# Kernel tuning notes

Hardware: AMD Instinct MI355X
Metric: run time of the kernel (lower is better)

## Reference

```python
import jax, jax.numpy as jnp
import numpy as np

H = 16  # num_heads
D = 1024  # hidden_size

def setup_inputs() -> dict:
    key = jax.random.key(0)
    ks = jax.random.split(key, 9)
    s = 1.0 / np.sqrt(D).astype(np.float32)
    return {
        'x':  jax.random.normal(ks[0], (2, 2048, D), dtype=jnp.float32),
        'wq': jax.random.normal(ks[1], (D, D), dtype=jnp.float32) * s,
        'bq': jax.random.normal(ks[2], (D,), dtype=jnp.float32) * s,
        'wk': jax.random.normal(ks[3], (D, D), dtype=jnp.float32) * s,
        'bk': jax.random.normal(ks[4], (D,), dtype=jnp.float32) * s,
        'wv': jax.random.normal(ks[5], (D, D), dtype=jnp.float32) * s,
        'bv': jax.random.normal(ks[6], (D,), dtype=jnp.float32) * s,
        'wo': jax.random.normal(ks[7], (D, D), dtype=jnp.float32) * s,
        'bo': jax.random.normal(ks[8], (D,), dtype=jnp.float32) * s,
    }

def _split_heads(t):
    # [b, s, (h d)] -> [b, h, s, d]
    b, s, _ = t.shape
    return t.reshape(b, s, H, D // H).transpose(0, 2, 1, 3)

def reference(x, wq, bq, wk, bk, wv, bv, wo, bo):
    q = _split_heads(x @ wq + bq)  # [b, h, s, d]
    k = _split_heads(x @ wk + bk)
    v = _split_heads(x @ wv + bv)
    scale = 1.0 / jnp.sqrt(jnp.asarray(q.shape[-1], q.dtype))
    attn = jnp.einsum('bhqd,bhkd->bhqk', q, k) * scale
    attn = jax.nn.softmax(attn, axis=-1)
    o = jnp.einsum('bhqk,bhkd->bhqd', attn, v)
    b, h, s, d = o.shape
    o = o.transpose(0, 2, 1, 3).reshape(b, s, h * d)  # concat heads
    return o @ wo + bo
```

## Files before the change

kernel.cpp:

```cpp
#include <hip/hip_runtime.h>
#include <stdint.h>
#include <stddef.h>


typedef __bf16 bf16_t;
typedef __bf16 bf16x8 __attribute__((ext_vector_type(8)));
typedef __bf16 bf16x4 __attribute__((ext_vector_type(4)));
typedef __bf16 bf16x2 __attribute__((ext_vector_type(2)));
typedef float  f32x4  __attribute__((ext_vector_type(4)));
typedef float  f32x8  __attribute__((ext_vector_type(8)));
typedef float  f32x16 __attribute__((ext_vector_type(16)));
typedef uint32_t u32x4 __attribute__((ext_vector_type(4)));

static constexpr float kQScale = 0.18033688011112042f;

__device__ __forceinline__ void gload_lds16(const bf16_t* g, bf16_t* l) {
  __builtin_amdgcn_global_load_lds((__attribute__((address_space(1))) void*)(void*)g,
                                   (__attribute__((address_space(3))) void*)l, 16, 0, 0);
}

__device__ __forceinline__ uint32_t pk_bf16(float lo, float hi) {
  bf16x2 v; v[0] = (bf16_t)lo; v[1] = (bf16_t)hi;
  return __builtin_bit_cast(uint32_t, v);
}

__global__ __launch_bounds__(256) void prep_k(
    const float* __restrict__ x, bf16_t* __restrict__ xb,
    const float* __restrict__ wq, const float* __restrict__ wk,
    const float* __restrict__ wv, const float* __restrict__ wo,
    bf16_t* __restrict__ wqkvT, bf16_t* __restrict__ woT) {
  __shared__ float t[64][65];
  const int z = blockIdx.z;
  if (z == 4) {
    const int blk = blockIdx.y * 16 + blockIdx.x;
#pragma unroll
    for (int c = 0; c < 16; ++c) {
      const int i = c * 65536 + blk * 256 + threadIdx.x;
      float4 v = ((const float4*)x)[i];
      bf16x4 o;
      o[0] = (bf16_t)v.x; o[1] = (bf16_t)v.y; o[2] = (bf16_t)v.z; o[3] = (bf16_t)v.w;
      ((bf16x4*)xb)[i] = o;
    }
    return;
  }
  const float* src = z == 0 ? wq : z == 1 ? wk : z == 2 ? wv : wo;
  bf16_t* dst = z < 3 ? wqkvT + (size_t)z * 1024 * 1024 : woT;
  int n0 = blockIdx.x * 64, k0 = blockIdx.y * 64;
  int c = threadIdx.x & 63, r4 = threadIdx.x >> 6;
#pragma unroll
  for (int i = 0; i < 16; ++i) {
    int r = r4 + i * 4;
    t[r][c] = src[(size_t)(k0 + r) * 1024 + (n0 + c)];
  }
  __syncthreads();
#pragma unroll
  for (int i = 0; i < 16; ++i) {
    int r = r4 + i * 4;
    dst[(size_t)(n0 + r) * 1024 + (k0 + c)] = (bf16_t)t[c][r];
  }
}

__global__ __launch_bounds__(256) void gemm_qkv_k(
    const bf16_t* __restrict__ A, const bf16_t* __restrict__ Bw,
    bf16_t* __restrict__ Qb, bf16_t* __restrict__ Kb, bf16_t* __restrict__ Vt,
    const float* __restrict__ bq, const float* __restrict__ bk, const float* __restrict__ bv) {
  __shared__ alignas(16) bf16_t As[128 * 32];
  __shared__ alignas(16) bf16_t Bs[128 * 32];
  const int tid = threadIdx.x;
  const int lane = tid & 63;
  const int w = tid >> 6, wr = w >> 1, wc = w & 1;
  const int brow = blockIdx.y * 128, bcol = blockIdx.x * 128;
  const int l15 = lane & 15, ko = (lane >> 4) * 8;

  f32x4 acc[4][4] = {};
  const bf16_t* Ab = A + (size_t)brow * 1024;
  const bf16_t* Bb = Bw + (size_t)bcol * 1024;

  const int e0 = tid * 8;
  const int r0 = e0 >> 5, c0 = e0 & 31;

  for (int k0 = 0; k0 < 1024; k0 += 32) {
    gload_lds16(Ab + (size_t)r0 * 1024 + k0 + c0, &As[e0]);
    gload_lds16(Ab + (size_t)(r0 + 64) * 1024 + k0 + c0, &As[e0 + 2048]);
    gload_lds16(Bb + (size_t)r0 * 1024 + k0 + c0, &Bs[e0]);
    gload_lds16(Bb + (size_t)(r0 + 64) * 1024 + k0 + c0, &Bs[e0 + 2048]);
    __syncthreads();
    bf16x8 af[4], bfg[4];
#pragma unroll
    for (int i = 0; i < 4; ++i)
      af[i] = *(const bf16x8*)&As[(wr * 64 + i * 16 + l15) * 32 + ko];
#pragma unroll
    for (int i = 0; i < 4; ++i)
      bfg[i] = *(const bf16x8*)&Bs[(wc * 64 + i * 16 + l15) * 32 + ko];
#pragma unroll
    for (int i = 0; i < 4; ++i)
#pragma unroll
      for (int j = 0; j < 4; ++j)
        acc[i][j] = __builtin_amdgcn_mfma_f32_16x16x32_bf16(af[i], bfg[j], acc[i][j], 0, 0, 0);
    __syncthreads();
  }

  const int mat = bcol >> 10;
#pragma unroll
  for (int i = 0; i < 4; ++i) {
    const int gm0 = brow + wr * 64 + i * 16 + ((lane >> 4) << 2);
    const int b = gm0 >> 11, s0 = gm0 & 2047;
#pragma unroll
    for (int j = 0; j < 4; ++j) {
      const int gn = bcol + wc * 64 + j * 16 + l15;
      const int col = gn & 1023;
      const int h = col >> 6, dd = col & 63;
      if (mat == 2) {
        const float bsv = bv[col];
        bf16x4 pk;
#pragma unroll
        for (int r = 0; r < 4; ++r) pk[r] = (bf16_t)(acc[i][j][r] + bsv);
        *(bf16x4*)&Vt[(((size_t)b * 16 + h) * 64 + dd) * 2048 + s0] = pk;
      } else {
        bf16_t* dst = mat == 0 ? Qb : Kb;
        const float bsv = (mat == 0 ? bq : bk)[col];
        const float scl = mat == 0 ? kQScale : 1.0f;
#pragma unroll
        for (int r = 0; r < 4; ++r)
          dst[((((size_t)b * 16 + h) * 2048 + (s0 + r)) * 64 + dd)] = (bf16_t)((acc[i][j][r] + bsv) * scl);
      }
    }
  }
}

__global__ __launch_bounds__(256) void gemm_out_k(
    const bf16_t* __restrict__ A, const bf16_t* __restrict__ Bw,
    float* __restrict__ outF, const float* __restrict__ bo) {
  __shared__ alignas(16) bf16_t As[128 * 32];
  __shared__ alignas(16) bf16_t Bs[64 * 32];
  const int tid = threadIdx.x;
  const int lane = tid & 63;
  const int w = tid >> 6;
  const int brow = blockIdx.y * 128, bcol = blockIdx.x * 64;
  const int l15 = lane & 15, ko = (lane >> 4) * 8;

  f32x4 acc[2][4] = {};
  const bf16_t* Ab = A + (size_t)brow * 1024;
  const bf16_t* Bb = Bw + (size_t)bcol * 1024;

  const int e0 = tid * 8;
  const int r0 = e0 >> 5, c0 = e0 & 31;

  for (int k0 = 0; k0 < 1024; k0 += 32) {
    gload_lds16(Ab + (size_t)r0 * 1024 + k0 + c0, &As[e0]);
    gload_lds16(Ab + (size_t)(r0 + 64) * 1024 + k0 + c0, &As[e0 + 2048]);
    gload_lds16(Bb + (size_t)r0 * 1024 + k0 + c0, &Bs[e0]);
    __syncthreads();
    bf16x8 af[2], bfg[4];
#pragma unroll
    for (int i = 0; i < 2; ++i)
      af[i] = *(const bf16x8*)&As[(w * 32 + i * 16 + l15) * 32 + ko];
#pragma unroll
    for (int j = 0; j < 4; ++j)
      bfg[j] = *(const bf16x8*)&Bs[(j * 16 + l15) * 32 + ko];
#pragma unroll
    for (int i = 0; i < 2; ++i)
#pragma unroll
      for (int j = 0; j < 4; ++j)
        acc[i][j] = __builtin_amdgcn_mfma_f32_16x16x32_bf16(af[i], bfg[j], acc[i][j], 0, 0, 0);
    __syncthreads();
  }

#pragma unroll
  for (int i = 0; i < 2; ++i) {
    const int gm0 = brow + w * 32 + i * 16 + ((lane >> 4) << 2);
#pragma unroll
    for (int j = 0; j < 4; ++j) {
      const int gn = bcol + j * 16 + l15;
      const float bsv = bo[gn];
#pragma unroll
      for (int r = 0; r < 4; ++r)
        outF[(size_t)(gm0 + r) * 1024 + gn] = acc[i][j][r] + bsv;
    }
  }
}

__global__ __launch_bounds__(512) void attn_k(
    const bf16_t* __restrict__ Qb, const bf16_t* __restrict__ Kb,
    const bf16_t* __restrict__ Vt, bf16_t* __restrict__ O) {
  __shared__ alignas(16) bf16_t Ksm[2][2][4096];
  __shared__ alignas(16) bf16_t Vsm[2][2][4096];
  const int tid = threadIdx.x, lane = tid & 63, w = tid >> 6;
  const int l31 = lane & 31, hi = lane >> 5;
  const int qsub = w & 3, half = w >> 2;
  const int work = (blockIdx.x & 7) * 32 + (blockIdx.x >> 3);
  const int bh = work >> 3;
  const int q0 = (work & 7) * 256 + qsub * 64;

  const bf16_t* Qp = Qb + ((size_t)bh * 2048 + q0) * 64;

  const int chunk0 = qsub * 64 + lane;
  const int srow = chunk0 >> 3;
  const int swzc = (chunk0 & 7) ^ (srow & 7);
  const char* srcK0 = (const char*)(Kb + ((size_t)bh * 2048 + half * 1024) * 64) + srow * 128 + swzc * 16;
  const char* srcK1 = srcK0 + 32 * 128;
  const char* srcV0 = (const char*)(Vt + (size_t)bh * 64 * 2048 + half * 1024) + srow * 4096 + swzc * 16;
  const char* srcV1 = srcV0 + 32 * 4096;

  auto stage = [&](int buf) {
    bf16_t* kb = &Ksm[half][buf][qsub * 512];
    bf16_t* vb = &Vsm[half][buf][qsub * 512];
    gload_lds16((const bf16_t*)srcK0, kb);
    gload_lds16((const bf16_t*)srcK1, kb + 2048);
    gload_lds16((const bf16_t*)srcV0, vb);
    gload_lds16((const bf16_t*)srcV1, vb + 2048);
    srcK0 += 8192; srcK1 += 8192;
    srcV0 += 128;  srcV1 += 128;
  };

  const int xorv = l31 & 7;
  const bf16_t* kcb[4];
#pragma unroll
  for (int j = 0; j < 4; ++j) {
    const int co = ((j * 2 + hi) ^ xorv) * 8;
    kcb[j] = &Ksm[half][0][l31 * 64 + co];
  }
  const bf16_t* vptr[8];
#pragma unroll
  for (int c = 0; c < 8; ++c)
    vptr[c] = &Vsm[half][0][l31 * 64 + ((c ^ xorv) << 3) + 4 * hi];

  bf16x8 qf[2][4];
#pragma unroll
  for (int qb = 0; qb < 2; ++qb)
#pragma unroll
    for (int ds = 0; ds < 4; ++ds)
      qf[qb][ds] = *(const bf16x8*)&Qp[(size_t)(qb * 32 + l31) * 64 + ds * 16 + hi * 8];

  f32x16 oA0 = {}, oA1 = {}, oB0 = {}, oB1 = {};
  float mxA = -1e30f, liA = 0.0f, mxB = -1e30f, liB = 0.0f;

  auto softmax_pack = [&](f32x16& s0, f32x16& s1, float& mx, float& li,
                          f32x16& oa, f32x16& ob, uint32_t* pw0, uint32_t* pw1) {
    f32x16 mm = __builtin_elementwise_max(s0, s1);
    f32x8 m8 = __builtin_elementwise_max(
        __builtin_shufflevector(mm, mm, 0, 1, 2, 3, 4, 5, 6, 7),
        __builtin_shufflevector(mm, mm, 8, 9, 10, 11, 12, 13, 14, 15));
    f32x4 m4 = __builtin_elementwise_max(
        __builtin_shufflevector(m8, m8, 0, 1, 2, 3),
        __builtin_shufflevector(m8, m8, 4, 5, 6, 7));
    float tmax = fmaxf(fmaxf(m4[0], m4[1]), fmaxf(m4[2], m4[3]));
    tmax = fmaxf(tmax, __shfl_xor(tmax, 32));
    if (__any(tmax > mx + 8.0f)) {
      const float mn = fmaxf(mx, tmax);
      const float corr = __builtin_amdgcn_exp2f(mx - mn);
      mx = mn;
      li *= corr;
      oa *= corr;
      ob *= corr;
    }
    s0 -= mx;
    s1 -= mx;
#pragma unroll
    for (int r = 0; r < 16; ++r) {
      s0[r] = __builtin_amdgcn_exp2f(s0[r]);
      s1[r] = __builtin_amdgcn_exp2f(s1[r]);
    }
    f32x16 sv = s0 + s1;
    f32x8 sv8 = __builtin_shufflevector(sv, sv, 0, 1, 2, 3, 4, 5, 6, 7) +
                __builtin_shufflevector(sv, sv, 8, 9, 10, 11, 12, 13, 14, 15);
    f32x4 sv4 = __builtin_shufflevector(sv8, sv8, 0, 1, 2, 3) +
                __builtin_shufflevector(sv8, sv8, 4, 5, 6, 7);
    float rs = (sv4[0] + sv4[1]) + (sv4[2] + sv4[3]);
    rs += __shfl_xor(rs, 32);
    li += rs;
#pragma unroll
    for (int g = 0; g < 4; ++g) {
      pw0[g * 2 + 0] = pk_bf16(s0[4 * g + 0], s0[4 * g + 1]);
      pw0[g * 2 + 1] = pk_bf16(s0[4 * g + 2], s0[4 * g + 3]);
      pw1[g * 2 + 0] = pk_bf16(s1[4 * g + 0], s1[4 * g + 1]);
      pw1[g * 2 + 1] = pk_bf16(s1[4 * g + 2], s1[4 * g + 3]);
    }
  };

  auto tile_body = [&](int buf) {
    const int bo = buf * 4096;
    bf16x8 kf0[4], kf1[4];
#pragma unroll
    for (int ds = 0; ds < 4; ++ds) {
      kf0[ds] = *(const bf16x8*)(kcb[ds] + bo);
      kf1[ds] = *(const bf16x8*)(kcb[ds] + bo + 2048);
    }
    f32x16 sA0 = {}, sA1 = {}, sB0 = {}, sB1 = {};
    __builtin_amdgcn_s_setprio(1);
#pragma unroll
    for (int ds = 0; ds < 4; ++ds) {
      sA0 = __builtin_amdgcn_mfma_f32_32x32x16_bf16(kf0[ds], qf[0][ds], sA0, 0, 0, 0);
      sB0 = __builtin_amdgcn_mfma_f32_32x32x16_bf16(kf0[ds], qf[1][ds], sB0, 0, 0, 0);
    }
#pragma unroll
    for (int ds = 0; ds < 4; ++ds) {
      sA1 = __builtin_amdgcn_mfma_f32_32x32x16_bf16(kf1[ds], qf[0][ds], sA1, 0, 0, 0);
      sB1 = __builtin_amdgcn_mfma_f32_32x32x16_bf16(kf1[ds], qf[1][ds], sB1, 0, 0, 0);
    }
    __builtin_amdgcn_s_setprio(0);

    uint32_t pwA0[8], pwA1[8], pwB0[8], pwB1[8];
    softmax_pack(sA0, sA1, mxA, liA, oA0, oA1, pwA0, pwA1);
    softmax_pack(sB0, sB1, mxB, liB, oB0, oB1, pwB0, pwB1);

#pragma unroll
    for (int st = 0; st < 2; ++st) {
#pragma unroll
      for (int ks = 0; ks < 2; ++ks) {
        const bf16_t* pA = vptr[4 * st + 2 * ks] + bo;
        const bf16_t* pB = vptr[4 * st + 2 * ks + 1] + bo;
        const bf16x4 a0 = *(const bf16x4*)pA;
        const bf16x4 a1 = *(const bf16x4*)pB;
        const bf16x4 b0 = *(const bf16x4*)(pA + 2048);
        const bf16x4 b1 = *(const bf16x4*)(pB + 2048);
        const bf16x8 v0 = __builtin_shufflevector(a0, a1, 0, 1, 2, 3, 4, 5, 6, 7);
        const bf16x8 v1 = __builtin_shufflevector(b0, b1, 0, 1, 2, 3, 4, 5, 6, 7);
        const uint32_t* pwA = st ? pwA1 : pwA0;
        const uint32_t* pwB = st ? pwB1 : pwB0;
        u32x4 fa, fb;
        fa[0] = pwA[4 * ks + 0]; fa[1] = pwA[4 * ks + 1];
        fa[2] = pwA[4 * ks + 2]; fa[3] = pwA[4 * ks + 3];
        fb[0] = pwB[4 * ks + 0]; fb[1] = pwB[4 * ks + 1];
        fb[2] = pwB[4 * ks + 2]; fb[3] = pwB[4 * ks + 3];
        const bf16x8 pfA = __builtin_bit_cast(bf16x8, fa);
        const bf16x8 pfB = __builtin_bit_cast(bf16x8, fb);
        __builtin_amdgcn_s_setprio(1);
        oA0 = __builtin_amdgcn_mfma_f32_32x32x16_bf16(v0, pfA, oA0, 0, 0, 0);
        oA1 = __builtin_amdgcn_mfma_f32_32x32x16_bf16(v1, pfA, oA1, 0, 0, 0);
        oB0 = __builtin_amdgcn_mfma_f32_32x32x16_bf16(v0, pfB, oB0, 0, 0, 0);
        oB1 = __builtin_amdgcn_mfma_f32_32x32x16_bf16(v1, pfB, oB1, 0, 0, 0);
        __builtin_amdgcn_s_setprio(0);
      }
    }
  };

  stage(0);
  __syncthreads();
#pragma unroll 1
  for (int t = 0; t < 16; t += 2) {
    stage(1);
    tile_body(0);
    __syncthreads();
    if (t + 2 < 16) stage(0);
    tile_body(1);
    if (t + 2 < 16) __syncthreads();
  }

  __syncthreads();
  float* cmb_o  = (float*)&Ksm[0][0][0];
  float* cmb_ml = (float*)&Vsm[0][0][0];
  const int b = bh >> 4, h = bh & 15;

  if (half) {
    cmb_ml[((0 * 2 + 0) * 4 + qsub) * 64 + lane] = mxA;
    cmb_ml[((0 * 2 + 1) * 4 + qsub) * 64 + lane] = liA;
    cmb_ml[((1 * 2 + 0) * 4 + qsub) * 64 + lane] = mxB;
    cmb_ml[((1 * 2 + 1) * 4 + qsub) * 64 + lane] = liB;
#pragma unroll
    for (int r = 0; r < 16; ++r) {
      cmb_o[(qsub * 32 + r) * 64 + lane] = oA0[r];
      cmb_o[(qsub * 32 + 16 + r) * 64 + lane] = oA1[r];
    }
  }
  __syncthreads();
  if (!half) {
    const float mb = cmb_ml[((0 * 2 + 0) * 4 + qsub) * 64 + lane];
    const float lb = cmb_ml[((0 * 2 + 1) * 4 + qsub) * 64 + lane];
    const float M = fmaxf(mxA, mb);
    const float ca = __builtin_amdgcn_exp2f(mxA - M);
    const float cb = __builtin_amdgcn_exp2f(mb - M);
    const float L = liA * ca + lb * cb;
    const float inv = 1.0f / L;
    const float fa = ca * inv, fb = cb * inv;
    const size_t row = (size_t)b * 2048 + q0 + l31;
#pragma unroll
    for (int g = 0; g < 4; ++g) {
      bf16x4 p0, p1;
#pragma unroll
      for (int r = 0; r < 4; ++r) {
        p0[r] = (bf16_t)(oA0[4 * g + r] * fa + cmb_o[(qsub * 32 + 4 * g + r) * 64 + lane] * fb);
        p1[r] = (bf16_t)(oA1[4 * g + r] * fa + cmb_o[(qsub * 32 + 16 + 4 * g + r) * 64 + lane] * fb);
      }
      *(bf16x4*)&O[row * 1024 + h * 64 + 0  + g * 8 + hi * 4] = p0;
      *(bf16x4*)&O[row * 1024 + h * 64 + 32 + g * 8 + hi * 4] = p1;
    }
  }
  __syncthreads();
  if (half) {
#pragma unroll
    for (int r = 0; r < 16; ++r) {
      cmb_o[(qsub * 32 + r) * 64 + lane] = oB0[r];
      cmb_o[(qsub * 32 + 16 + r) * 64 + lane] = oB1[r];
    }
  }
  __syncthreads();
  if (!half) {
    const float mb = cmb_ml[((1 * 2 + 0) * 4 + qsub) * 64 + lane];
    const float lb = cmb_ml[((1 * 2 + 1) * 4 + qsub) * 64 + lane];
    const float M = fmaxf(mxB, mb);
    const float ca = __builtin_amdgcn_exp2f(mxB - M);
    const float cb = __builtin_amdgcn_exp2f(mb - M);
    const float L = liB * ca + lb * cb;
    const float inv = 1.0f / L;
    const float fa = ca * inv, fb = cb * inv;
    const size_t row = (size_t)b * 2048 + q0 + 32 + l31;
#pragma unroll
    for (int g = 0; g < 4; ++g) {
      bf16x4 p0, p1;
#pragma unroll
      for (int r = 0; r < 4; ++r) {
        p0[r] = (bf16_t)(oB0[4 * g + r] * fa + cmb_o[(qsub * 32 + 4 * g + r) * 64 + lane] * fb);
        p1[r] = (bf16_t)(oB1[4 * g + r] * fa + cmb_o[(qsub * 32 + 16 + 4 * g + r) * 64 + lane] * fb);
      }
      *(bf16x4*)&O[row * 1024 + h * 64 + 0  + g * 8 + hi * 4] = p0;
      *(bf16x4*)&O[row * 1024 + h * 64 + 32 + g * 8 + hi * 4] = p1;
    }
  }
}

extern "C" void kernel_launch(void* const* d_in, const int* in_sizes, int n_in,
                              void* d_out, int out_size, void* d_ws, size_t ws_size,
                              hipStream_t stream) {
  const float* x  = (const float*)d_in[0];
  const float* wq = (const float*)d_in[1];
  const float* bq = (const float*)d_in[2];
  const float* wk = (const float*)d_in[3];
  const float* bk = (const float*)d_in[4];
  const float* wv = (const float*)d_in[5];
  const float* bv = (const float*)d_in[6];
  const float* wo = (const float*)d_in[7];
  const float* bo = (const float*)d_in[8];
  float* out = (float*)d_out;

  if (ws_size < ((size_t)48 << 20)) return;
  char* ws = (char*)d_ws;
  bf16_t* xb  = (bf16_t*)(ws);
  bf16_t* wT  = (bf16_t*)(ws + ((size_t)8 << 20));
  bf16_t* woT = wT + (size_t)3072 * 1024;
  bf16_t* Qb  = (bf16_t*)(ws + ((size_t)16 << 20));
  bf16_t* Kb  = (bf16_t*)(ws + ((size_t)24 << 20));
  bf16_t* Vt  = (bf16_t*)(ws + ((size_t)32 << 20));
  bf16_t* O   = xb;

  prep_k<<<dim3(16, 16, 5), 256, 0, stream>>>(x, xb, wq, wk, wv, wo, wT, woT);
  gemm_qkv_k<<<dim3(24, 32), 256, 0, stream>>>(xb, wT, Qb, Kb, Vt, bq, bk, bv);
  attn_k<<<256, 512, 0, stream>>>(Qb, Kb, Vt, O);
  gemm_out_k<<<dim3(16, 32), 256, 0, stream>>>(O, woT, out, bo);
}
```

Measured before the change: 116.7 us.

## Split attention KV range four ways per block and double grid size

Each attention block now covers 128 queries instead of 256, and its 8 waves split the 2048 keys into four quarters of 512 instead of two halves. The grid doubles to 512 blocks. The K/V double buffering is dropped: each iteration stages one tile, syncs, computes, then syncs again. At the end, three quarters' partial softmax state is merged through LDS. The aim is more blocks for better CU occupancy, in exchange for losing load/compute overlap, adding more barriers and a heavier cross-wave combine.

```diff
diff --git a/kernel.cpp b/kernel.cpp
--- a/kernel.cpp
+++ b/kernel.cpp
@@ -183,47 +183,52 @@
 __global__ __launch_bounds__(512) void attn_k(
     const bf16_t* __restrict__ Qb, const bf16_t* __restrict__ Kb,
     const bf16_t* __restrict__ Vt, bf16_t* __restrict__ O) {
-  __shared__ alignas(16) bf16_t Ksm[2][2][4096];
-  __shared__ alignas(16) bf16_t Vsm[2][2][4096];
+  __shared__ alignas(16) char smem[65536];
   const int tid = threadIdx.x, lane = tid & 63, w = tid >> 6;
   const int l31 = lane & 31, hi = lane >> 5;
-  const int qsub = w & 3, half = w >> 2;
-  const int work = (blockIdx.x & 7) * 32 + (blockIdx.x >> 3);
-  const int bh = work >> 3;
-  const int q0 = (work & 7) * 256 + qsub * 64;
+  const int qsub = w & 1, quarter = w >> 1;
+  const int work = (blockIdx.x & 7) * 64 + (blockIdx.x >> 3);
+  const int bh = work >> 4;
+  const int q0 = (work & 15) * 128 + qsub * 64;
+
+  bf16_t* Ksm = (bf16_t*)(smem + quarter * 16384);
+  bf16_t* Vsm = (bf16_t*)(smem + quarter * 16384 + 8192);
 
   const bf16_t* Qp = Qb + ((size_t)bh * 2048 + q0) * 64;
 
-  const int chunk0 = qsub * 64 + lane;
-  const int srow = chunk0 >> 3;
-  const int swzc = (chunk0 & 7) ^ (srow & 7);
-  const char* srcK0 = (const char*)(Kb + ((size_t)bh * 2048 + half * 1024) * 64) + srow * 128 + swzc * 16;
-  const char* srcK1 = srcK0 + 32 * 128;
-  const char* srcV0 = (const char*)(Vt + (size_t)bh * 64 * 2048 + half * 1024) + srow * 4096 + swzc * 16;
-  const char* srcV1 = srcV0 + 32 * 4096;
-
-  auto stage = [&](int buf) {
-    bf16_t* kb = &Ksm[half][buf][qsub * 512];
-    bf16_t* vb = &Vsm[half][buf][qsub * 512];
-    gload_lds16((const bf16_t*)srcK0, kb);
-    gload_lds16((const bf16_t*)srcK1, kb + 2048);
-    gload_lds16((const bf16_t*)srcV0, vb);
-    gload_lds16((const bf16_t*)srcV1, vb + 2048);
-    srcK0 += 8192; srcK1 += 8192;
-    srcV0 += 128;  srcV1 += 128;
+  const int lrow = lane >> 3;
+  const int swz = (lane & 7) ^ lrow;
+  const char* baseK = (const char*)(Kb + ((size_t)bh * 2048 + quarter * 512) * 64);
+  const char* baseV = (const char*)(Vt + (size_t)bh * 64 * 2048 + quarter * 512);
+  const char* srcK[4];
+  const char* srcV[4];
+#pragma unroll
+  for (int i = 0; i < 4; ++i) {
+    srcK[i] = baseK + (qsub * 8 + i * 16 + lrow) * 128 + swz * 16;
+    srcV[i] = baseV + (size_t)(qsub * 8 + i * 16 + lrow) * 4096 + swz * 16;
+  }
+
+  auto stage = [&]() {
+    bf16_t* kb = Ksm + qsub * 512;
+    bf16_t* vb = Vsm + qsub * 512;
+#pragma unroll
+    for (int i = 0; i < 4; ++i) {
+      gload_lds16((const bf16_t*)srcK[i], kb + i * 1024);
+      gload_lds16((const bf16_t*)srcV[i], vb + i * 1024);
+      srcK[i] += 8192;
+      srcV[i] += 128;
+    }
   };
 
   const int xorv = l31 & 7;
   const bf16_t* kcb[4];
-#pragma unroll
-  for (int j = 0; j < 4; ++j) {
-    const int co = ((j * 2 + hi) ^ xorv) * 8;
-    kcb[j] = &Ksm[half][0][l31 * 64 + co];
-  }
   const bf16_t* vptr[8];
 #pragma unroll
+  for (int j = 0; j < 4; ++j)
+    kcb[j] = &Ksm[l31 * 64 + ((j * 2 + hi) ^ xorv) * 8];
+#pragma unroll
   for (int c = 0; c < 8; ++c)
-    vptr[c] = &Vsm[half][0][l31 * 64 + ((c ^ xorv) << 3) + 4 * hi];
+    vptr[c] = &Vsm[l31 * 64 + ((c ^ xorv) << 3) + 4 * hi];
 
   bf16x8 qf[2][4];
 #pragma unroll
@@ -278,13 +283,12 @@
     }
   };
 
-  auto tile_body = [&](int buf) {
-    const int bo = buf * 4096;
+  auto tile_body = [&]() {
     bf16x8 kf0[4], kf1[4];
 #pragma unroll
     for (int ds = 0; ds < 4; ++ds) {
-      kf0[ds] = *(const bf16x8*)(kcb[ds] + bo);
-      kf1[ds] = *(const bf16x8*)(kcb[ds] + bo + 2048);
+      kf0[ds] = *(const bf16x8*)(kcb[ds]);
+      kf1[ds] = *(const bf16x8*)(kcb[ds] + 2048);
     }
     f32x16 sA0 = {}, sA1 = {}, sB0 = {}, sB1 = {};
     __builtin_amdgcn_s_setprio(1);
@@ -308,8 +312,8 @@
     for (int st = 0; st < 2; ++st) {
 #pragma unroll
       for (int ks = 0; ks < 2; ++ks) {
-        const bf16_t* pA = vptr[4 * st + 2 * ks] + bo;
-        const bf16_t* pB = vptr[4 * st + 2 * ks + 1] + bo;
+        const bf16_t* pA = vptr[4 * st + 2 * ks];
+        const bf16_t* pB = vptr[4 * st + 2 * ks + 1];
         const bf16x4 a0 = *(const bf16x4*)pA;
         const bf16x4 a1 = *(const bf16x4*)pB;
         const bf16x4 b0 = *(const bf16x4*)(pA + 2048);
@@ -335,83 +339,102 @@
     }
   };
 
-  stage(0);
+#pragma unroll 1
+  for (int t = 0; t < 8; ++t) {
+    stage();
+    __syncthreads();
+    tile_body();
+    __syncthreads();
+  }
+
+  float* scr = (float*)smem;
+  float* sml = scr + 12288;
+  const int b = bh >> 4, h = bh & 15;
+
+  if (quarter != 0) {
+    const int r3 = (quarter - 1) * 2 + qsub;
+    sml[r3 * 128 + lane] = mxA;
+    sml[r3 * 128 + 64 + lane] = liA;
+#pragma unroll
+    for (int r = 0; r < 16; ++r) {
+      scr[(r3 * 32 + r) * 64 + lane] = oA0[r];
+      scr[(r3 * 32 + 16 + r) * 64 + lane] = oA1[r];
+    }
+  }
   __syncthreads();
-#pragma unroll 1
-  for (int t = 0; t < 16; t += 2) {
-    stage(1);
-    tile_body(0);
-    __syncthreads();
-    if (t + 2 < 16) stage(0);
-    tile_body(1);
-    if (t + 2 < 16) __syncthreads();
-  }
-
-  __syncthreads();
-  float* cmb_o  = (float*)&Ksm[0][0][0];
-  float* cmb_ml = (float*)&Vsm[0][0][0];
-  const int b = bh >> 4, h = bh & 15;
-
-  if (half) {
-    cmb_ml[((0 * 2 + 0) * 4 + qsub) * 64 + lane] = mxA;
-    cmb_ml[((0 * 2 + 1) * 4 + qsub) * 64 + lane] = liA;
-    cmb_ml[((1 * 2 + 0) * 4 + qsub) * 64 + lane] = mxB;
-    cmb_ml[((1 * 2 + 1) * 4 + qsub) * 64 + lane] = liB;
-#pragma unroll
-    for (int r = 0; r < 16; ++r) {
-      cmb_o[(qsub * 32 + r) * 64 + lane] = oA0[r];
-      cmb_o[(qsub * 32 + 16 + r) * 64 + lane] = oA1[r];
-    }
-  }
-  __syncthreads();
-  if (!half) {
-    const float mb = cmb_ml[((0 * 2 + 0) * 4 + qsub) * 64 + lane];
-    const float lb = cmb_ml[((0 * 2 + 1) * 4 + qsub) * 64 + lane];
-    const float M = fmaxf(mxA, mb);
-    const float ca = __builtin_amdgcn_exp2f(mxA - M);
-    const float cb = __builtin_amdgcn_exp2f(mb - M);
-    const float L = liA * ca + lb * cb;
+  if (quarter == 0) {
+    float M = mxA, L = liA;
+    f32x16 t0 = oA0, t1 = oA1;
+#pragma unroll
+    for (int qt = 1; qt < 4; ++qt) {
+      const int r3 = (qt - 1) * 2 + qsub;
+      const float m2 = sml[r3 * 128 + lane];
+      const float l2 = sml[r3 * 128 + 64 + lane];
+      const float Mn = fmaxf(M, m2);
+      const float ca = __builtin_amdgcn_exp2f(M - Mn);
+      const float cb = __builtin_amdgcn_exp2f(m2 - Mn);
+      L = L * ca + l2 * cb;
+      M = Mn;
+#pragma unroll
+      for (int r = 0; r < 16; ++r) {
+        t0[r] = t0[r] * ca + scr[(r3 * 32 + r) * 64 + lane] * cb;
+        t1[r] = t1[r] * ca + scr[(r3 * 32 + 16 + r) * 64 + lane] * cb;
+      }
+    }
     const float inv = 1.0f / L;
-    const float fa = ca * inv, fb = cb * inv;
     const size_t row = (size_t)b * 2048 + q0 + l31;
 #pragma unroll
     for (int g = 0; g < 4; ++g) {
       bf16x4 p0, p1;
 #pragma unroll
       for (int r = 0; r < 4; ++r) {
-        p0[r] = (bf16_t)(oA0[4 * g + r] * fa + cmb_o[(qsub * 32 + 4 * g + r) * 64 + lane] * fb);
-        p1[r] = (bf16_t)(oA1[4 * g + r] * fa + cmb_o[(qsub * 32 + 16 + 4 * g + r) * 64 + lane] * fb);
+        p0[r] = (bf16_t)(t0[4 * g + r] * inv);
+        p1[r] = (bf16_t)(t1[4 * g + r] * inv);
       }
       *(bf16x4*)&O[row * 1024 + h * 64 + 0  + g * 8 + hi * 4] = p0;
       *(bf16x4*)&O[row * 1024 + h * 64 + 32 + g * 8 + hi * 4] = p1;
     }
   }
   __syncthreads();
-  if (half) {
+  if (quarter != 0) {
+    const int r3 = (quarter - 1) * 2 + qsub;
+    sml[r3 * 128 + lane] = mxB;
+    sml[r3 * 128 + 64 + lane] = liB;
 #pragma unroll
     for (int r = 0; r < 16; ++r) {
-      cmb_o[(qsub * 32 + r) * 64 + lane] = oB0[r];
-      cmb_o[(qsub * 32 + 16 + r) * 64 + lane] = oB1[r];
+      scr[(r3 * 32 + r) * 64 + lane] = oB0[r];
+      scr[(r3 * 32 + 16 + r) * 64 + lane] = oB1[r];
     }
   }
   __syncthreads();
-  if (!half) {
-    const float mb = cmb_ml[((1 * 2 + 0) * 4 + qsub) * 64 + lane];
-    const float lb = cmb_ml[((1 * 2 + 1) * 4 + qsub) * 64 + lane];
-    const float M = fmaxf(mxB, mb);
-    const float ca = __builtin_amdgcn_exp2f(mxB - M);
-    const float cb = __builtin_amdgcn_exp2f(mb - M);
-    const float L = liB * ca + lb * cb;
+  if (quarter == 0) {
+    float M = mxB, L = liB;
+    f32x16 t0 = oB0, t1 = oB1;
+#pragma unroll
+    for (int qt = 1; qt < 4; ++qt) {
+      const int r3 = (qt - 1) * 2 + qsub;
+      const float m2 = sml[r3 * 128 + lane];
+      const float l2 = sml[r3 * 128 + 64 + lane];
+      const float Mn = fmaxf(M, m2);
+      const float ca = __builtin_amdgcn_exp2f(M - Mn);
+      const float cb = __builtin_amdgcn_exp2f(m2 - Mn);
+      L = L * ca + l2 * cb;
+      M = Mn;
+#pragma unroll
+      for (int r = 0; r < 16; ++r) {
+        t0[r] = t0[r] * ca + scr[(r3 * 32 + r) * 64 + lane] * cb;
+        t1[r] = t1[r] * ca + scr[(r3 * 32 + 16 + r) * 64 + lane] * cb;
+      }
+    }
     const float inv = 1.0f / L;
-    const float fa = ca * inv, fb = cb * inv;
     const size_t row = (size_t)b * 2048 + q0 + 32 + l31;
 #pragma unroll
     for (int g = 0; g < 4; ++g) {
       bf16x4 p0, p1;
 #pragma unroll
       for (int r = 0; r < 4; ++r) {
-        p0[r] = (bf16_t)(oB0[4 * g + r] * fa + cmb_o[(qsub * 32 + 4 * g + r) * 64 + lane] * fb);
-        p1[r] = (bf16_t)(oB1[4 * g + r] * fa + cmb_o[(qsub * 32 + 16 + 4 * g + r) * 64 + lane] * fb);
+        p0[r] = (bf16_t)(t0[4 * g + r] * inv);
+        p1[r] = (bf16_t)(t1[4 * g + r] * inv);
       }
       *(bf16x4*)&O[row * 1024 + h * 64 + 0  + g * 8 + hi * 4] = p0;
       *(bf16x4*)&O[row * 1024 + h * 64 + 32 + g * 8 + hi * 4] = p1;
@@ -445,6 +468,6 @@
 
   prep_k<<<dim3(16, 16, 5), 256, 0, stream>>>(x, xb, wq, wk, wv, wo, wT, woT);
   gemm_qkv_k<<<dim3(24, 32), 256, 0, stream>>>(xb, wT, Qb, Kb, Vt, bq, bk, bv);
-  attn_k<<<256, 512, 0, stream>>>(Qb, Kb, Vt, O);
+  attn_k<<<512, 512, 0, stream>>>(Qb, Kb, Vt, O);
   gemm_out_k<<<dim3(16, 32), 256, 0, stream>>>(O, woT, out, bo);
 }
```

After: 128.0 us. +9.7%, slower.
